# Kernel tuning notes

Hardware: AMD Instinct MI355X
Metric: run time of the kernel (lower is better)

## Reference

```python
import jax, jax.numpy as jnp
import numpy as np

B, N, F, D, H, L, K = 128, 128, 13, 256, 8, 8, 10
FF = 2 * D  # FFN / hidden width
HEAD = D // H


def setup_inputs() -> dict:
    key = jax.random.key(0)
    ks = iter(jax.random.split(key, 64))
    def nrm(shape, scale=0.02):
        return jax.random.normal(next(ks), shape, dtype=jnp.float32) * scale
    return {
        "input_features": jax.random.normal(next(ks), (B, N, F), dtype=jnp.float32),
        "input_points": jax.random.normal(next(ks), (B, N, 2), dtype=jnp.float32),
        "input_mask": jnp.ones((B, N, 1), dtype=jnp.float32),
        "input_time": jax.random.uniform(next(ks), (B, 1), dtype=jnp.float32),
        # get_encoding: Dense(2D, gelu) -> Dense(D, gelu)
        "enc_w1": nrm((F, FF)), "enc_b1": jnp.zeros((FF,), jnp.float32),
        "enc_w2": nrm((FF, D)), "enc_b2": jnp.zeros((D,), jnp.float32),
        # FourierProjection MLP (no bias, swish)
        "four_w1": nrm((D, FF)), "four_w2": nrm((FF, D)),
        # FiLM time projection (no bias)
        "time_w": nrm((D, FF)),
        # local KNN MLPs: round 0 input 2*F, round 1 input 2*D
        "loc1_w1": nrm((2 * F, FF)), "loc1_b1": jnp.zeros((FF,), jnp.float32),
        "loc1_w2": nrm((FF, D)), "loc1_b2": jnp.zeros((D,), jnp.float32),
        "loc2_w1": nrm((2 * D, FF)), "loc2_b1": jnp.zeros((FF,), jnp.float32),
        "loc2_w2": nrm((FF, D)), "loc2_b2": jnp.zeros((D,), jnp.float32),
        # transformer encoder layers, stacked over L
        "qkv_w": nrm((L, D, 3 * D)), "qkv_b": jnp.zeros((L, 3 * D), jnp.float32),
        "out_w": nrm((L, D, D)), "out_b": jnp.zeros((L, D), jnp.float32),
        "ln1_g": jnp.ones((L, D), jnp.float32), "ln1_b": jnp.zeros((L, D), jnp.float32),
        "ff1_w": nrm((L, D, FF)), "ff1_b": jnp.zeros((L, FF), jnp.float32),
        "ff2_w": nrm((L, FF, D)), "ff2_b": jnp.zeros((L, D), jnp.float32),
        "gamma": jnp.full((L, D), 1e-5, dtype=jnp.float32),
        "ln2_g": jnp.ones((L, D), jnp.float32), "ln2_b": jnp.zeros((L, D), jnp.float32),
    }


def _ln(x, g, b, eps=1e-5):
    m = jnp.mean(x, axis=-1, keepdims=True)
    v = jnp.var(x, axis=-1, keepdims=True)
    return (x - m) * jax.lax.rsqrt(v + eps) * g + b


def _fourier(t, w1, w2):
    # t: (B,1) -> (B,D)
    half = D // 2
    emb = np.log(10000.0) / (half - 1)
    freq = jnp.exp(-emb * jnp.arange(half, dtype=jnp.float32))
    angle = t * freq[None, :] * 1000.0  # (B, half)
    e = jnp.concatenate([jnp.sin(angle), jnp.cos(angle)], axis=-1)
    e = jax.nn.silu(e @ w1)
    return jax.nn.silu(e @ w2)


def _get_neighbors(points, feats, w1, b1, w2, b2):
    # points: (B,N,P), feats: (B,N,C) -> (B,N,D)
    r = jnp.sum(points * points, axis=-1)  # (B,N)
    d = r[:, :, None] - 2.0 * jnp.einsum('bnp,bmp->bnm', points, points) + r[:, None, :]
    _, idx = jax.lax.top_k(-d, K + 1)
    idx = idx[:, :, 1:]  # drop self, (B,N,K)
    knn = jax.vmap(lambda f, i: f[i])(feats, idx)  # (B,N,K,C)
    center = jnp.broadcast_to(feats[:, :, None, :], knn.shape)
    local = jnp.concatenate([knn - center, center], axis=-1)  # (B,N,K,2C)
    local = jax.nn.gelu(local @ w1 + b1)
    local = jax.nn.gelu(local @ w2 + b2)
    return jnp.mean(local, axis=2)


def _mha(x, mask, wqkv, bqkv, wo, bo):
    Bx, Nx, _ = x.shape
    qkv = x @ wqkv + bqkv
    q, k, v = jnp.split(qkv, 3, axis=-1)
    def heads(t):
        return t.reshape(Bx, Nx, H, HEAD).transpose(0, 2, 1, 3)
    q, k, v = heads(q), heads(k), heads(v)
    scores = jnp.einsum('bhqd,bhkd->bhqk', q, k) * (1.0 / np.sqrt(HEAD))
    keep = mask[:, None, None, :, 0] > 0  # (B,1,1,N)
    scores = jnp.where(keep, scores, -1e9)
    a = jax.nn.softmax(scores, axis=-1)
    o = jnp.einsum('bhqk,bhkd->bhqd', a, v).transpose(0, 2, 1, 3).reshape(Bx, Nx, D)
    return o @ wo + bo


def _pet(input_features, input_points, input_mask, input_time,
         enc_w1, enc_b1, enc_w2, enc_b2, four_w1, four_w2, time_w,
         loc1_w1, loc1_b1, loc1_w2, loc1_b2, loc2_w1, loc2_b1, loc2_w2, loc2_b2,
         qkv_w, qkv_b, out_w, out_b, ln1_g, ln1_b, ff1_w, ff1_b, ff2_w, ff2_b,
         gamma, ln2_g, ln2_b):
    # feature encoding (RandomDrop is identity at eval / feature_drop=0)
    enc = jax.nn.gelu(input_features @ enc_w1 + enc_b1)
    enc = jax.nn.gelu(enc @ enc_w2 + enc_b2)  # (B,N,D)
    # FiLM time conditioning
    t = _fourier(input_time, four_w1, four_w2)  # (B,D)
    t = t[:, None, :] * input_mask  # (B,N,D)
    scale, shift = jnp.split(t @ time_w, 2, axis=-1)
    enc = enc * (1.0 + scale) + shift
    # local KNN aggregation
    coord_shift = 999.0 * (1.0 - input_mask)  # (B,N,1)
    points = input_points[:, :, :2]
    lf = _get_neighbors(coord_shift + points, input_features, loc1_w1, loc1_b1, loc1_w2, loc1_b2)
    lf = _get_neighbors(coord_shift + lf, lf, loc2_w1, loc2_b1, loc2_w2, loc2_b2)
    enc = enc + lf
    skip = enc
    x = enc
    for i in range(L):
        res = x
        a = _mha(x, input_mask, qkv_w[i], qkv_b[i], out_w[i], out_b[i])
        x = _ln(res + a, ln1_g[i], ln1_b[i])
        res = x
        h = jax.nn.gelu(x @ ff1_w[i] + ff1_b[i])
        h = h @ ff2_w[i] + ff2_b[i]
        h = h * gamma[i] * input_mask  # LayerScale with mask
        x = _ln(res + h, ln2_g[i], ln2_b[i])
    return x + skip


def reference(input_features, input_points, input_mask, input_time,
              enc_w1, enc_b1, enc_w2, enc_b2, four_w1, four_w2, time_w,
              loc1_w1, loc1_b1, loc1_w2, loc1_b2, loc2_w1, loc2_b1, loc2_w2, loc2_b2,
              qkv_w, qkv_b, out_w, out_b, ln1_g, ln1_b, ff1_w, ff1_b, ff2_w, ff2_b,
              gamma, ln2_g, ln2_b):
    return _pet(input_features, input_points, input_mask, input_time,
                enc_w1, enc_b1, enc_w2, enc_b2, four_w1, four_w2, time_w,
                loc1_w1, loc1_b1, loc1_w2, loc1_b2, loc2_w1, loc2_b1, loc2_w2, loc2_b2,
                qkv_w, qkv_b, out_w, out_b, ln1_g, ln1_b, ff1_w, ff1_b, ff2_w, ff2_b,
                gamma, ln2_g, ln2_b)
```

## Files before the change

kernel.cpp:

```cpp
#include <hip/hip_runtime.h>
#include <hip/hip_bf16.h>
#include <cmath>

#define DEV_INLINE __device__ __forceinline__

constexpr int Bn = 128;
constexpr int Nn = 128;
constexpr int Fn = 13;
constexpr int Dn = 256;
constexpr int Ln = 8;
constexpr int Kn = 10;
constexpr int FFn = 512;
constexpr int Tn = Bn * Nn;
constexpr int Rn = Tn * Kn;

typedef __attribute__((ext_vector_type(4))) float f32x4;
typedef __attribute__((ext_vector_type(8))) short bf16x8;
typedef unsigned short us;

__device__ float g_x[Tn * Dn];
__device__ float g_skip[Tn * Dn];
__device__ float g_big[Tn * Dn];
__device__ float g_dm[Tn * Nn];
__device__ float g_u[Bn * FFn];
__device__ float g_r[Tn];
__device__ float g_pqbias[2048];
__device__ int   g_idx[Rn];
__device__ us g_bigb[Tn * 768];
__device__ us g_xb[Tn * Dn];
__device__ us g_attb[Tn * Dn];
__device__ us g_lf1b[Tn * Dn];
__device__ us g_pq[Tn * 1024];
__device__ us g_h2b[Rn * Dn];
__device__ us g_feat16[Tn * 32];
constexpr int OFF_ENC1 = 0;
constexpr int OFF_ENC2 = OFF_ENC1 + 512 * 32;
constexpr int OFF_W2A  = OFF_ENC2 + 256 * 512;
constexpr int OFF_W2B  = OFF_W2A + 256 * 512;
constexpr int OFF_PQ1  = OFF_W2B + 256 * 512;
constexpr int OFF_PQ2  = OFF_PQ1 + 1024 * 32;
constexpr int OFF_QKV  = OFF_PQ2 + 1024 * 256;
constexpr int OFF_OUT  = OFF_QKV + 8 * 768 * 256;
constexpr int OFF_FF1  = OFF_OUT + 8 * 256 * 256;
constexpr int OFF_FF2  = OFF_FF1 + 8 * 512 * 256;
constexpr int WT_TOTAL = OFF_FF2 + 8 * 256 * 512;
__device__ us g_wt[WT_TOTAL];

DEV_INLINE float gelu_f(float x) {
    float x2 = x * x;
    float m = x * fmaf(x2, -0.07135537f, -1.59576912f);
    float t = __expf(m);
    return x * __builtin_amdgcn_rcpf(1.f + t);
}
DEV_INLINE us f2b(float x) {
    __hip_bfloat16 h = __float2bfloat16(x);
    return *(us*)&h;
}
DEV_INLINE float blo(unsigned u) { return __uint_as_float(u << 16); }
DEV_INLINE float bhi(unsigned u) { return __uint_as_float(u & 0xFFFF0000u); }
DEV_INLINE unsigned pk2(float a, float b) {
    float2 f; f.x = a; f.y = b;
    __hip_bfloat162 h = __float22bfloat162_rn(f);
    return *(unsigned*)&h;
}

#define GLOAD16(gp, lp)                                                            \
    __builtin_amdgcn_global_load_lds(                                              \
        (const __attribute__((address_space(1))) unsigned int*)(gp),               \
        (__attribute__((address_space(3))) unsigned int*)(lp), 16, 0, 0)

constexpr int UP0 = 0;
constexpr int UP1 = UP0 + 16;
constexpr int UP2 = UP1 + 128;
constexpr int UP3 = UP2 + 128;
constexpr int UP4 = UP3 + 128;
constexpr int UP5 = UP4 + 1536;
constexpr int UP6 = UP5 + 512;
constexpr int UP7 = UP6 + 1024;
constexpr int UP8 = UP7 + 1024;
constexpr int UP9 = UP8 + 1024;
constexpr int UP10 = UP9 + 1024;
constexpr int UP11 = UP10 + 2048;
constexpr int UP12 = UP11 + 128;
constexpr int UPN = UP12 + 128;

DEV_INLINE void prep_seg(const float* __restrict__ src, us* __restrict__ dst,
                         int Kreal, int Kpad, int Nd, long sstride, long dstride,
                         int gx, int gy, int lb, int tid, float* tile) {
    int z = lb / (gx * gy);
    int rem = lb - z * gx * gy;
    int by = rem / gx, bx = rem - by * gx;
    const float* s = src + (size_t)z * sstride;
    us* d = dst + (size_t)z * dstride;
    int cn = tid & 31, rk = tid >> 5;
    int kbase = by * 32, nbase = bx * 32;
#pragma unroll
    for (int p = 0; p < 4; p++) {
        int k = kbase + p * 8 + rk;
        float v = (k < Kreal) ? s[(size_t)k * Nd + nbase + cn] : 0.f;
        tile[(p * 8 + rk) * 33 + cn] = v;
    }
    __syncthreads();
#pragma unroll
    for (int p = 0; p < 4; p++) {
        int nl = p * 8 + rk;
        d[(size_t)(nbase + nl) * Kpad + kbase + cn] = f2b(tile[cn * 33 + nl]);
    }
}

DEV_INLINE void prepPQ_seg(const float* __restrict__ w1, const float* __restrict__ b1,
                           us* __restrict__ dst, float* __restrict__ bdst,
                           int Kreal, int Kpad, int n, int tid) {
    for (int k = tid; k < Kpad; k += 256) {
        float v;
        if (n < 512) v = (k < Kreal) ? w1[(size_t)k * 512 + n] : 0.f;
        else {
            int m = n - 512;
            v = (k < Kreal) ? (w1[(size_t)(Kreal + k) * 512 + m] - w1[(size_t)k * 512 + m]) : 0.f;
        }
        dst[(size_t)n * Kpad + k] = f2b(v);
    }
    if (tid == 0) bdst[n] = (n < 512) ? 0.f : b1[n - 512];
}

__global__ __launch_bounds__(256) void k_uprep(
    const float* __restrict__ enc_w1, const float* __restrict__ enc_w2,
    const float* __restrict__ l1w2, const float* __restrict__ l2w2,
    const float* __restrict__ qkv_w, const float* __restrict__ out_w,
    const float* __restrict__ ff1w, const float* __restrict__ ff2w,
    const float* __restrict__ l1w1, const float* __restrict__ l1b1,
    const float* __restrict__ l2w1, const float* __restrict__ l2b1,
    const float* __restrict__ feat, const float* __restrict__ tin,
    const float* __restrict__ four_w1, const float* __restrict__ four_w2,
    const float* __restrict__ time_w, const float* __restrict__ pts,
    const float* __restrict__ mask,
    us* __restrict__ wt, float* __restrict__ pqbias, us* __restrict__ fp,
    float* __restrict__ u, int* __restrict__ idx) {
    __shared__ float shmem[1056];
    int b = blockIdx.x, tid = threadIdx.x;
    if (b < UP1) {
        prep_seg(enc_w1, wt + OFF_ENC1, 13, 32, 512, 0, 0, 16, 1, b - UP0, tid, shmem);
    } else if (b < UP2) {
        prep_seg(enc_w2, wt + OFF_ENC2, 512, 512, 256, 0, 0, 8, 16, b - UP1, tid, shmem);
    } else if (b < UP3) {
        prep_seg(l1w2, wt + OFF_W2A, 512, 512, 256, 0, 0, 8, 16, b - UP2, tid, shmem);
    } else if (b < UP4) {
        prep_seg(l2w2, wt + OFF_W2B, 512, 512, 256, 0, 0, 8, 16, b - UP3, tid, shmem);
    } else if (b < UP5) {
        prep_seg(qkv_w, wt + OFF_QKV, 256, 256, 768, 256 * 768, 768 * 256, 24, 8, b - UP4, tid, shmem);
    } else if (b < UP6) {
        prep_seg(out_w, wt + OFF_OUT, 256, 256, 256, 256 * 256, 256 * 256, 8, 8, b - UP5, tid, shmem);
    } else if (b < UP7) {
        prep_seg(ff1w, wt + OFF_FF1, 256, 256, 512, 256 * 512, 512 * 256, 16, 8, b - UP6, tid, shmem);
    } else if (b < UP8) {
        prep_seg(ff2w, wt + OFF_FF2, 512, 512, 256, 512 * 256, 256 * 512, 8, 16, b - UP7, tid, shmem);
    } else if (b < UP9) {
        prepPQ_seg(l1w1, l1b1, wt + OFF_PQ1, pqbias, 13, 32, b - UP8, tid);
    } else if (b < UP10) {
        prepPQ_seg(l2w1, l2b1, wt + OFF_PQ2, pqbias + 1024, 256, 256, b - UP9, tid);
    } else if (b < UP11) {
        int gid = (b - UP10) * 256 + tid;
        int t = gid >> 5, c = gid & 31;
        fp[gid] = (c < Fn) ? f2b(feat[(size_t)t * Fn + c]) : (us)0;
    } else if (b < UP12) {
        float* e = shmem; float* e1 = shmem + 256; float* t2 = shmem + 768;
        int bb = b - UP11;
        float tv = tin[bb];
        if (tid < 128) {
            const float emb = 0.07252236513366287f;
            float fr = expf(-emb * (float)tid);
            float ang = tv * fr * 1000.f;
            e[tid] = sinf(ang);
            e[tid + 128] = cosf(ang);
        }
        __syncthreads();
        for (int j = tid; j < 512; j += 256) {
            float s = 0.f;
            for (int i = 0; i < 256; i++) s += e[i] * four_w1[(size_t)i * 512 + j];
            e1[j] = s / (1.f + expf(-s));
        }
        __syncthreads();
        {
            float s = 0.f;
            for (int i = 0; i < 512; i++) s += e1[i] * four_w2[(size_t)i * 256 + tid];
            t2[tid] = s / (1.f + expf(-s));
        }
        __syncthreads();
        for (int j = tid; j < 512; j += 256) {
            float s = 0.f;
            for (int i = 0; i < 256; i++) s += t2[i] * time_w[(size_t)i * 512 + j];
            u[(size_t)bb * 512 + j] = s;
        }
    } else {
        float* px = shmem; float* py = shmem + 128; float* rr = shmem + 256;
        int bb = b - UP12;
        if (tid < 128) {
            int n = tid;
            float shift = 999.f * (1.f - mask[bb * Nn + n]);
            float x = pts[(size_t)(bb * Nn + n) * 2 + 0] + shift;
            float y = pts[(size_t)(bb * Nn + n) * 2 + 1] + shift;
            px[n] = x; py[n] = y; rr[n] = x * x + y * y;
        }
        __syncthreads();
        if (tid < 128) {
            int n = tid;
            float x = px[n], y = py[n], rn = rr[n];
            float bd[Kn + 1]; int bi[Kn + 1];
#pragma unroll
            for (int j = 0; j <= Kn; j++) { bd[j] = 3.4e38f; bi[j] = -1; }
            for (int m = 0; m < Nn; m++) {
                float d = rn - 2.f * (x * px[m] + y * py[m]) + rr[m];
                if (d < bd[Kn]) {
                    int j = Kn;
                    while (j > 0 && d < bd[j - 1]) { bd[j] = bd[j - 1]; bi[j] = bi[j - 1]; j--; }
                    bd[j] = d; bi[j] = m;
                }
            }
            for (int j = 1; j <= Kn; j++) idx[(size_t)(bb * Nn + n) * Kn + j - 1] = bi[j];
        }
    }
}

template <int EPI, bool OBF>
__global__ __launch_bounds__(256) void k_mg2(const us* __restrict__ A,
                                             const us* __restrict__ Bt,
                                             const float* __restrict__ bias,
                                             void* __restrict__ Cp,
                                             int Kd, int Nd) {
    __shared__ __align__(16) us As[128 * 32];
    __shared__ __align__(16) us Bs[128 * 32];
    int tid = threadIdx.x;
    int m0 = blockIdx.y << 7, n0 = blockIdx.x << 7;
    int wave = tid >> 6, lane = tid & 63;
    int wm = (wave & 1) << 6, wn = (wave >> 1) << 6;
    int lm = lane & 15, quad = lane >> 4;
    int r0 = (wave << 5) + (lane >> 2);
    int colu = (((lane & 3) ^ ((lane >> 2) & 3)) << 3);
    const us* pa0 = A + (size_t)(m0 + r0) * Kd + colu;
    const us* pa1 = A + (size_t)(m0 + r0 + 16) * Kd + colu;
    const us* pb0 = Bt + (size_t)(n0 + r0) * Kd + colu;
    const us* pb1 = Bt + (size_t)(n0 + r0 + 16) * Kd + colu;
    auto lAs = (__attribute__((address_space(3))) us*)As;
    auto lBs = (__attribute__((address_space(3))) us*)Bs;
    int lbase = wave << 10;
    int fcol = ((quad ^ (lm & 3)) << 3);
    f32x4 acc[4][4] = {};
    for (int k0 = 0; k0 < Kd; k0 += 32) {
        __syncthreads();
        GLOAD16(pa0 + k0, lAs + lbase);
        GLOAD16(pa1 + k0, lAs + lbase + 512);
        GLOAD16(pb0 + k0, lBs + lbase);
        GLOAD16(pb1 + k0, lBs + lbase + 512);
        __syncthreads();
        bf16x8 afr[4], bfr[4];
#pragma unroll
        for (int i = 0; i < 4; i++) {
            afr[i] = *(const bf16x8*)&As[(wm + i * 16 + lm) * 32 + fcol];
            bfr[i] = *(const bf16x8*)&Bs[(wn + i * 16 + lm) * 32 + fcol];
        }
#pragma unroll
        for (int mf = 0; mf < 4; mf++)
#pragma unroll
            for (int nf = 0; nf < 4; nf++)
                acc[mf][nf] = __builtin_amdgcn_mfma_f32_16x16x32_bf16(afr[mf], bfr[nf], acc[mf][nf], 0, 0, 0);
    }
    float bvs[4];
#pragma unroll
    for (int nf = 0; nf < 4; nf++) bvs[nf] = bias[n0 + wn + nf * 16 + lm];
#pragma unroll
    for (int mf = 0; mf < 4; mf++) {
#pragma unroll
        for (int r = 0; r < 4; r++) {
            size_t row = (size_t)(m0 + wm + mf * 16 + (quad << 2) + r);
#pragma unroll
            for (int nf = 0; nf < 4; nf++) {
                float v = acc[mf][nf][r] + bvs[nf];
                if (EPI == 1) v = gelu_f(v);
                size_t ci = row * Nd + n0 + wn + nf * 16 + lm;
                if constexpr (OBF) ((us*)Cp)[ci] = f2b(v);
                else ((float*)Cp)[ci] = v;
            }
        }
    }
}

template <bool PM, bool FINAL>
__global__ __launch_bounds__(512) void k_mgln(const us* __restrict__ A,
                                              const us* __restrict__ Bt,
                                              const float* __restrict__ bias,
                                              const us* __restrict__ res,
                                              const float* __restrict__ gamma,
                                              const float* __restrict__ mask,
                                              const float* __restrict__ lng,
                                              const float* __restrict__ lnb,
                                              const float* __restrict__ skip,
                                              us* __restrict__ xbout,
                                              float* __restrict__ finout,
                                              int Kd) {
    __shared__ __align__(16) us As[64 * 32];
    __shared__ __align__(16) us Bs[256 * 32];
    __shared__ float2 part[8][64];
    __shared__ float2 stat[64];
    int tid = threadIdx.x;
    int m0 = blockIdx.x << 6;
    int wave = tid >> 6, lane = tid & 63;
    int wn = wave << 5;
    int lm = lane & 15, quad = lane >> 4;
    int colu = (((lane & 3) ^ ((lane >> 2) & 3)) << 3);
    int ar = (wave << 4) + (lane >> 2);
    int br = (wave << 5) + (lane >> 2);
    const us* pa = A + (size_t)(m0 + ar) * Kd + colu;
    const us* pb0 = Bt + (size_t)br * Kd + colu;
    const us* pb1 = Bt + (size_t)(br + 16) * Kd + colu;
    auto lAs = (__attribute__((address_space(3))) us*)As;
    auto lBs = (__attribute__((address_space(3))) us*)Bs;
    int fcol = ((quad ^ (lm & 3)) << 3);
    f32x4 acc[4][2] = {};
    for (int k0 = 0; k0 < Kd; k0 += 32) {
        __syncthreads();
        if (wave < 4) GLOAD16(pa + k0, lAs + (wave << 9));
        GLOAD16(pb0 + k0, lBs + (wave << 10));
        GLOAD16(pb1 + k0, lBs + (wave << 10) + 512);
        __syncthreads();
        bf16x8 afr[4], bfr[2];
#pragma unroll
        for (int i = 0; i < 4; i++)
            afr[i] = *(const bf16x8*)&As[(i * 16 + lm) * 32 + fcol];
#pragma unroll
        for (int j = 0; j < 2; j++)
            bfr[j] = *(const bf16x8*)&Bs[(wn + j * 16 + lm) * 32 + fcol];
#pragma unroll
        for (int mf = 0; mf < 4; mf++)
#pragma unroll
            for (int nf = 0; nf < 2; nf++)
                acc[mf][nf] = __builtin_amdgcn_mfma_f32_16x16x32_bf16(afr[mf], bfr[nf], acc[mf][nf], 0, 0, 0);
    }
    float bvs[2], gms[2];
#pragma unroll
    for (int nf = 0; nf < 2; nf++) {
        int col = wn + nf * 16 + lm;
        bvs[nf] = bias[col];
        if (PM) gms[nf] = gamma[col];
    }
#pragma unroll
    for (int mf = 0; mf < 4; mf++) {
#pragma unroll
        for (int r = 0; r < 4; r++) {
            int rowl = mf * 16 + (quad << 2) + r;
            size_t row = (size_t)(m0 + rowl);
            float mrow = PM ? mask[row] : 0.f;
            float s1 = 0.f, s2 = 0.f;
#pragma unroll
            for (int nf = 0; nf < 2; nf++) {
                int col = wn + nf * 16 + lm;
                float rv = blo((unsigned)res[row * 256 + col]);
                float v = acc[mf][nf][r] + bvs[nf];
                v = PM ? fmaf(v * gms[nf], mrow, rv) : rv + v;
                acc[mf][nf][r] = v;
                s1 += v; s2 += v * v;
            }
            s1 += __shfl_xor(s1, 1, 64); s2 += __shfl_xor(s2, 1, 64);
            s1 += __shfl_xor(s1, 2, 64); s2 += __shfl_xor(s2, 2, 64);
            s1 += __shfl_xor(s1, 4, 64); s2 += __shfl_xor(s2, 4, 64);
            s1 += __shfl_xor(s1, 8, 64); s2 += __shfl_xor(s2, 8, 64);
            if (lm == 0) { float2 p; p.x = s1; p.y = s2; part[wave][rowl] = p; }
        }
    }
    __syncthreads();
    if (tid < 64) {
        float s = 0.f, q = 0.f;
#pragma unroll
        for (int w = 0; w < 8; w++) { float2 p = part[w][tid]; s += p.x; q += p.y; }
        float mean = s * (1.f / 256.f);
        float var = q * (1.f / 256.f) - mean * mean;
        float2 st; st.x = mean; st.y = rsqrtf(var + 1e-5f);
        stat[tid] = st;
    }
    __syncthreads();
    float gvs[2], bts[2];
#pragma unroll
    for (int nf = 0; nf < 2; nf++) {
        int col = wn + nf * 16 + lm;
        gvs[nf] = lng[col];
        bts[nf] = lnb[col];
    }
#pragma unroll
    for (int mf = 0; mf < 4; mf++) {
#pragma unroll
        for (int r = 0; r < 4; r++) {
            int rowl = mf * 16 + (quad << 2) + r;
            size_t row = (size_t)(m0 + rowl);
            float2 st = stat[rowl];
#pragma unroll
            for (int nf = 0; nf < 2; nf++) {
                int col = wn + nf * 16 + lm;
                float nv = fmaf((acc[mf][nf][r] - st.x) * st.y, gvs[nf], bts[nf]);
                if (FINAL) finout[row * 256 + col] = nv + skip[row * 256 + col];
                else xbout[row * 256 + col] = f2b(nv);
            }
        }
    }
}

__global__ __launch_bounds__(512) void k_knng(const us* __restrict__ pq,
                                              const int* __restrict__ idx,
                                              const us* __restrict__ Bt,
                                              const float* __restrict__ bias,
                                              us* __restrict__ h2b) {
    __shared__ __align__(16) us As[128 * 64];
    __shared__ __align__(16) us Bs[256 * 64];
    int tid = threadIdx.x;
    int m0 = blockIdx.x << 7;
    int wave = tid >> 6, lane = tid & 63;
    int wm = (wave & 1) << 6, wn = (wave >> 1) << 6;
    int lm = lane & 15, quad = lane >> 4;
    int arow = tid >> 2, acolu = (tid & 3) << 4;
    int asw = arow & 7;
    int ablk0 = ((tid & 3) << 1) ^ asw, ablk1 = (((tid & 3) << 1) + 1) ^ asw;
    int r = m0 + arow;
    int tok = r / 10;
    int nb = idx[r];
    int prow = (tok & ~127) + nb;
    const us* Pp = pq + (size_t)prow * 1024 + acolu;
    const us* Qp = pq + (size_t)tok * 1024 + 512 + acolu;
    int brow = (wave << 5) + (lane >> 3);
    int bcol = (((lane & 7) ^ (lane >> 3)) << 3);
    const us* pb = Bt + (size_t)brow * 512 + bcol;
    auto lBs = (__attribute__((address_space(3))) us*)Bs;
    int lbase = wave << 11;
    int fsw = lm & 7;
    f32x4 acc[4][4] = {};
    for (int k0 = 0; k0 < 512; k0 += 64) {
        uint4 pv0 = *(const uint4*)(Pp + k0);
        uint4 pv1 = *(const uint4*)(Pp + k0 + 8);
        uint4 qv0 = *(const uint4*)(Qp + k0);
        uint4 qv1 = *(const uint4*)(Qp + k0 + 8);
        uint4 h0, h1;
        h0.x = pk2(gelu_f(blo(pv0.x) + blo(qv0.x)), gelu_f(bhi(pv0.x) + bhi(qv0.x)));
        h0.y = pk2(gelu_f(blo(pv0.y) + blo(qv0.y)), gelu_f(bhi(pv0.y) + bhi(qv0.y)));
        h0.z = pk2(gelu_f(blo(pv0.z) + blo(qv0.z)), gelu_f(bhi(pv0.z) + bhi(qv0.z)));
        h0.w = pk2(gelu_f(blo(pv0.w) + blo(qv0.w)), gelu_f(bhi(pv0.w) + bhi(qv0.w)));
        h1.x = pk2(gelu_f(blo(pv1.x) + blo(qv1.x)), gelu_f(bhi(pv1.x) + bhi(qv1.x)));
        h1.y = pk2(gelu_f(blo(pv1.y) + blo(qv1.y)), gelu_f(bhi(pv1.y) + bhi(qv1.y)));
        h1.z = pk2(gelu_f(blo(pv1.z) + blo(qv1.z)), gelu_f(bhi(pv1.z) + bhi(qv1.z)));
        h1.w = pk2(gelu_f(blo(pv1.w) + blo(qv1.w)), gelu_f(bhi(pv1.w) + bhi(qv1.w)));
        __syncthreads();
        GLOAD16(pb + k0, lBs + lbase);
        GLOAD16(pb + k0 + 8 * 512, lBs + lbase + 512);
        GLOAD16(pb + k0 + 16 * 512, lBs + lbase + 1024);
        GLOAD16(pb + k0 + 24 * 512, lBs + lbase + 1536);
        *(uint4*)&As[arow * 64 + (ablk0 << 3)] = h0;
        *(uint4*)&As[arow * 64 + (ablk1 << 3)] = h1;
        __syncthreads();
#pragma unroll
        for (int sub = 0; sub < 2; sub++) {
            int lblk = (sub << 2) + quad;
            int fcol = ((lblk ^ fsw) << 3);
            bf16x8 afr[4], bfr[4];
#pragma unroll
            for (int i = 0; i < 4; i++) {
                afr[i] = *(const bf16x8*)&As[(wm + i * 16 + lm) * 64 + fcol];
                bfr[i] = *(const bf16x8*)&Bs[(wn + i * 16 + lm) * 64 + fcol];
            }
#pragma unroll
            for (int mf = 0; mf < 4; mf++)
#pragma unroll
                for (int nf = 0; nf < 4; nf++)
                    acc[mf][nf] = __builtin_amdgcn_mfma_f32_16x16x32_bf16(afr[mf], bfr[nf], acc[mf][nf], 0, 0, 0);
        }
    }
    float bvs[4];
#pragma unroll
    for (int nf = 0; nf < 4; nf++) bvs[nf] = bias[wn + nf * 16 + lm];
#pragma unroll
    for (int mf = 0; mf < 4; mf++) {
#pragma unroll
        for (int rr = 0; rr < 4; rr++) {
            size_t row = (size_t)(m0 + wm + mf * 16 + (quad << 2) + rr);
#pragma unroll
            for (int nf = 0; nf < 4; nf++) {
                float v = gelu_f(acc[mf][nf][rr] + bvs[nf]);
                h2b[row * 256 + wn + nf * 16 + lm] = f2b(v);
            }
        }
    }
}

__global__ __launch_bounds__(64) void k_mean1s(const us* __restrict__ h2b,
                                               const float* __restrict__ mask,
                                               us* __restrict__ lfb,
                                               float* __restrict__ big,
                                               float* __restrict__ r) {
    int t = blockIdx.x, lane = threadIdx.x;
    int c = lane << 2;
    const us* p = h2b + (size_t)t * Kn * 256 + c;
    float s0 = 0.f, s1 = 0.f, s2 = 0.f, s3 = 0.f;
#pragma unroll
    for (int k = 0; k < Kn; k++) {
        uint2 v = *(const uint2*)(p + k * 256);
        s0 += blo(v.x); s1 += bhi(v.x);
        s2 += blo(v.y); s3 += bhi(v.y);
    }
    s0 *= 0.1f; s1 *= 0.1f; s2 *= 0.1f; s3 *= 0.1f;
    uint2 ob; ob.x = pk2(s0, s1); ob.y = pk2(s2, s3);
    *(uint2*)&lfb[(size_t)t * 256 + c] = ob;
    float sh = 999.f * (1.f - mask[t]);
    float4 w; w.x = s0 + sh; w.y = s1 + sh; w.z = s2 + sh; w.w = s3 + sh;
    *(float4*)&big[(size_t)t * 256 + c] = w;
    float sq = w.x * w.x + w.y * w.y + w.z * w.z + w.w * w.w;
#pragma unroll
    for (int off = 32; off; off >>= 1) sq += __shfl_xor(sq, off, 64);
    if (lane == 0) r[t] = sq;
}

__global__ __launch_bounds__(256) void k_dist(const float* __restrict__ fe,
                                              const float* __restrict__ r,
                                              float* __restrict__ Dm) {
    int b = blockIdx.z;
    int m0 = blockIdx.x * 64, n0 = blockIdx.y * 64;
    const float* A = fe + (size_t)b * Nn * Dn;
    __shared__ float As[16][68];
    __shared__ float Bs[16][68];
    int tid = threadIdx.x;
    int tx = tid & 15, ty = tid >> 4;
    int ar = tid >> 2, ac = (tid & 3) << 2;
    float acc[4][4] = {};
    for (int k0 = 0; k0 < Dn; k0 += 16) {
        float4 av = *(const float4*)&A[(size_t)(n0 + ar) * Dn + k0 + ac];
        float4 bv = *(const float4*)&A[(size_t)(m0 + ar) * Dn + k0 + ac];
        __syncthreads();
        As[ac + 0][ar] = av.x; As[ac + 1][ar] = av.y; As[ac + 2][ar] = av.z; As[ac + 3][ar] = av.w;
        Bs[ac + 0][ar] = bv.x; Bs[ac + 1][ar] = bv.y; Bs[ac + 2][ar] = bv.z; Bs[ac + 3][ar] = bv.w;
        __syncthreads();
#pragma unroll
        for (int kk = 0; kk < 16; kk++) {
            float4 a = *(const float4*)&As[kk][ty << 2];
            float4 b2 = *(const float4*)&Bs[kk][tx << 2];
            acc[0][0] += a.x * b2.x; acc[0][1] += a.x * b2.y; acc[0][2] += a.x * b2.z; acc[0][3] += a.x * b2.w;
            acc[1][0] += a.y * b2.x; acc[1][1] += a.y * b2.y; acc[1][2] += a.y * b2.z; acc[1][3] += a.y * b2.w;
            acc[2][0] += a.z * b2.x; acc[2][1] += a.z * b2.y; acc[2][2] += a.z * b2.z; acc[2][3] += a.z * b2.w;
            acc[3][0] += a.w * b2.x; acc[3][1] += a.w * b2.y; acc[3][2] += a.w * b2.z; acc[3][3] += a.w * b2.w;
        }
    }
    float4 rm = *(const float4*)&r[b * Nn + m0 + (tx << 2)];
#pragma unroll
    for (int i = 0; i < 4; i++) {
        int n = n0 + (ty << 2) + i;
        float rn = r[b * Nn + n];
        float4 v;
        v.x = rn - 2.f * acc[i][0] + rm.x;
        v.y = rn - 2.f * acc[i][1] + rm.y;
        v.z = rn - 2.f * acc[i][2] + rm.z;
        v.w = rn - 2.f * acc[i][3] + rm.w;
        *(float4*)&Dm[(size_t)b * Nn * Nn + (size_t)n * Nn + m0 + (tx << 2)] = v;
    }
}

__global__ __launch_bounds__(128) void k_topkg(const float* __restrict__ Dm, int* __restrict__ idx) {
    int b = blockIdx.x, n = threadIdx.x;
    const float* row = Dm + (size_t)b * Nn * Nn + (size_t)n * Nn;
    float bd[Kn + 1]; int bi[Kn + 1];
#pragma unroll
    for (int j = 0; j <= Kn; j++) { bd[j] = 3.4e38f; bi[j] = -1; }
    for (int m = 0; m < Nn; m++) {
        float d = row[m];
        if (d < bd[Kn]) {
            int j = Kn;
            while (j > 0 && d < bd[j - 1]) { bd[j] = bd[j - 1]; bi[j] = bi[j - 1]; j--; }
            bd[j] = d; bi[j] = m;
        }
    }
    for (int j = 1; j <= Kn; j++) idx[(size_t)(b * Nn + n) * Kn + j - 1] = bi[j];
}

__global__ __launch_bounds__(256) void k_meanc(const us* __restrict__ h2b,
                                               const float* __restrict__ u,
                                               const float* __restrict__ mask,
                                               const float* __restrict__ x,
                                               float* __restrict__ skip,
                                               us* __restrict__ xb) {
    int t = blockIdx.x, c = threadIdx.x;
    const us* p = h2b + (size_t)t * Kn * 256 + c;
    float s = 0.f;
#pragma unroll
    for (int k = 0; k < Kn; k++) s += blo((unsigned)p[k * 256]);
    s *= 0.1f;
    int b = t >> 7;
    float m = mask[t];
    float xv = x[(size_t)t * Dn + c];
    float sc = u[(size_t)b * 512 + c];
    float sh = u[(size_t)b * 512 + 256 + c];
    float v = xv * (1.f + m * sc) + m * sh + s;
    skip[(size_t)t * Dn + c] = v;
    xb[(size_t)t * Dn + c] = f2b(v);
}

__global__ __launch_bounds__(256) void k_attn(const us* __restrict__ qkv,
                                              const float* __restrict__ mask,
                                              us* __restrict__ outp) {
    __shared__ __align__(16) us Qs[128 * 40];
    __shared__ __align__(16) us Ks[128 * 40];
    __shared__ __align__(16) us Vt[32 * 136];
    __shared__ __align__(16) us Ps[128 * 136];
    __shared__ float msk[128];
    int bh = blockIdx.x;
    int b = bh >> 3, h = bh & 7;
    int tid = threadIdx.x;
    int wave = tid >> 6, lane = tid & 63;
    int lm = lane & 15, quad = lane >> 4;
    int wm = wave << 5;
    {
        int row = tid >> 1, off = (tid & 1) << 4;
        const us* rp = qkv + (size_t)(b * 128 + row) * 768 + h * 32 + off;
        *(uint4*)&Qs[row * 40 + off] = *(const uint4*)(rp);
        *(uint4*)&Qs[row * 40 + off + 8] = *(const uint4*)(rp + 8);
        *(uint4*)&Ks[row * 40 + off] = *(const uint4*)(rp + 256);
        *(uint4*)&Ks[row * 40 + off + 8] = *(const uint4*)(rp + 264);
        union { uint4 u[2]; us s[16]; } tv;
        tv.u[0] = *(const uint4*)(rp + 512);
        tv.u[1] = *(const uint4*)(rp + 520);
#pragma unroll
        for (int j = 0; j < 16; j++) Vt[(off + j) * 136 + row] = tv.s[j];
        if (tid < 128) msk[tid] = mask[b * 128 + tid];
    }
    __syncthreads();
    f32x4 acc[2][8] = {};
    {
        bf16x8 aq[2];
#pragma unroll
        for (int mf = 0; mf < 2; mf++)
            aq[mf] = *(const bf16x8*)&Qs[(wm + mf * 16 + lm) * 40 + (quad << 3)];
#pragma unroll
        for (int nf = 0; nf < 8; nf++) {
            bf16x8 bk = *(const bf16x8*)&Ks[(nf * 16 + lm) * 40 + (quad << 3)];
            acc[0][nf] = __builtin_amdgcn_mfma_f32_16x16x32_bf16(aq[0], bk, acc[0][nf], 0, 0, 0);
            acc[1][nf] = __builtin_amdgcn_mfma_f32_16x16x32_bf16(aq[1], bk, acc[1][nf], 0, 0, 0);
        }
    }
    {
        const float sc = 0.17677669529663687f;
        float mkc[8];
#pragma unroll
        for (int nf = 0; nf < 8; nf++) mkc[nf] = msk[nf * 16 + lm];
#pragma unroll
        for (int mf = 0; mf < 2; mf++) {
#pragma unroll
            for (int nf = 0; nf < 8; nf++)
#pragma unroll
                for (int r = 0; r < 4; r++) {
                    float s = acc[mf][nf][r];
                    acc[mf][nf][r] = mkc[nf] > 0.f ? s * sc : -1.0e9f;
                }
#pragma unroll
            for (int r = 0; r < 4; r++) {
                float m = acc[mf][0][r];
#pragma unroll
                for (int nf = 1; nf < 8; nf++) m = fmaxf(m, acc[mf][nf][r]);
                m = fmaxf(m, __shfl_xor(m, 1, 64));
                m = fmaxf(m, __shfl_xor(m, 2, 64));
                m = fmaxf(m, __shfl_xor(m, 4, 64));
                m = fmaxf(m, __shfl_xor(m, 8, 64));
                float s = 0.f;
#pragma unroll
                for (int nf = 0; nf < 8; nf++) {
                    float p = __expf(acc[mf][nf][r] - m);
                    acc[mf][nf][r] = p;
                    s += p;
                }
                s += __shfl_xor(s, 1, 64);
                s += __shfl_xor(s, 2, 64);
                s += __shfl_xor(s, 4, 64);
                s += __shfl_xor(s, 8, 64);
                float linv = __builtin_amdgcn_rcpf(s);
                int prow = wm + mf * 16 + (quad << 2) + r;
#pragma unroll
                for (int nf = 0; nf < 8; nf++)
                    Ps[prow * 136 + nf * 16 + lm] = f2b(acc[mf][nf][r] * linv);
            }
        }
    }
    __syncthreads();
    f32x4 oacc[2][2] = {};
    for (int kt = 0; kt < 4; kt++) {
        bf16x8 ap[2], bv[2];
#pragma unroll
        for (int mf = 0; mf < 2; mf++)
            ap[mf] = *(const bf16x8*)&Ps[(wm + mf * 16 + lm) * 136 + kt * 32 + (quad << 3)];
#pragma unroll
        for (int nf = 0; nf < 2; nf++)
            bv[nf] = *(const bf16x8*)&Vt[(nf * 16 + lm) * 136 + kt * 32 + (quad << 3)];
#pragma unroll
        for (int mf = 0; mf < 2; mf++)
#pragma unroll
            for (int nf = 0; nf < 2; nf++)
                oacc[mf][nf] = __builtin_amdgcn_mfma_f32_16x16x32_bf16(ap[mf], bv[nf], oacc[mf][nf], 0, 0, 0);
    }
#pragma unroll
    for (int mf = 0; mf < 2; mf++)
#pragma unroll
        for (int r = 0; r < 4; r++) {
            int row = wm + mf * 16 + (quad << 2) + r;
#pragma unroll
            for (int nf = 0; nf < 2; nf++)
                outp[(size_t)(b * 128 + row) * 256 + h * 32 + nf * 16 + lm] = f2b(oacc[nf == 0 ? mf : mf][nf][r]);
        }
}

extern "C" void kernel_launch(void* const* d_in, const int* in_sizes, int n_in,
                              void* d_out, int out_size, void* d_ws, size_t ws_size,
                              hipStream_t stream) {
    (void)in_sizes; (void)n_in; (void)out_size; (void)d_ws; (void)ws_size;
    const float* f_feat = (const float*)d_in[0];
    const float* f_pts  = (const float*)d_in[1];
    const float* f_mask = (const float*)d_in[2];
    const float* f_time = (const float*)d_in[3];
    const float* enc_w1 = (const float*)d_in[4];
    const float* enc_b1 = (const float*)d_in[5];
    const float* enc_w2 = (const float*)d_in[6];
    const float* enc_b2 = (const float*)d_in[7];
    const float* four_w1 = (const float*)d_in[8];
    const float* four_w2 = (const float*)d_in[9];
    const float* time_w = (const float*)d_in[10];
    const float* l1w1 = (const float*)d_in[11];
    const float* l1b1 = (const float*)d_in[12];
    const float* l1w2 = (const float*)d_in[13];
    const float* l1b2 = (const float*)d_in[14];
    const float* l2w1 = (const float*)d_in[15];
    const float* l2b1 = (const float*)d_in[16];
    const float* l2w2 = (const float*)d_in[17];
    const float* l2b2 = (const float*)d_in[18];
    const float* qkv_w = (const float*)d_in[19];
    const float* qkv_b = (const float*)d_in[20];
    const float* out_w = (const float*)d_in[21];
    const float* out_b = (const float*)d_in[22];
    const float* ln1g = (const float*)d_in[23];
    const float* ln1b = (const float*)d_in[24];
    const float* ff1w = (const float*)d_in[25];
    const float* ff1b = (const float*)d_in[26];
    const float* ff2w = (const float*)d_in[27];
    const float* ff2b = (const float*)d_in[28];
    const float* gam  = (const float*)d_in[29];
    const float* ln2g = (const float*)d_in[30];
    const float* ln2b = (const float*)d_in[31];
    float* out = (float*)d_out;

    float *x, *skip, *big, *dm, *u, *r, *pqbias;
    int* idx;
    us *bigb, *xb, *attb, *lf1b, *pq, *h2b, *feat16, *wt;
    hipGetSymbolAddress((void**)&x,    HIP_SYMBOL(g_x));
    hipGetSymbolAddress((void**)&skip, HIP_SYMBOL(g_skip));
    hipGetSymbolAddress((void**)&big,  HIP_SYMBOL(g_big));
    hipGetSymbolAddress((void**)&dm,   HIP_SYMBOL(g_dm));
    hipGetSymbolAddress((void**)&u,    HIP_SYMBOL(g_u));
    hipGetSymbolAddress((void**)&r,    HIP_SYMBOL(g_r));
    hipGetSymbolAddress((void**)&pqbias, HIP_SYMBOL(g_pqbias));
    hipGetSymbolAddress((void**)&idx,  HIP_SYMBOL(g_idx));
    hipGetSymbolAddress((void**)&bigb, HIP_SYMBOL(g_bigb));
    hipGetSymbolAddress((void**)&xb,   HIP_SYMBOL(g_xb));
    hipGetSymbolAddress((void**)&attb, HIP_SYMBOL(g_attb));
    hipGetSymbolAddress((void**)&lf1b, HIP_SYMBOL(g_lf1b));
    hipGetSymbolAddress((void**)&pq,   HIP_SYMBOL(g_pq));
    hipGetSymbolAddress((void**)&h2b,  HIP_SYMBOL(g_h2b));
    hipGetSymbolAddress((void**)&feat16, HIP_SYMBOL(g_feat16));
    hipGetSymbolAddress((void**)&wt,   HIP_SYMBOL(g_wt));

    k_uprep<<<UPN, 256, 0, stream>>>(
        enc_w1, enc_w2, l1w2, l2w2, qkv_w, out_w, ff1w, ff2w,
        l1w1, l1b1, l2w1, l2b1, f_feat, f_time, four_w1, four_w2, time_w,
        f_pts, f_mask, wt, pqbias, feat16, u, idx);

    k_mg2<1, true><<<dim3(4, 128), 256, 0, stream>>>(feat16, wt + OFF_ENC1, enc_b1, bigb, 32, 512);
    k_mg2<1, false><<<dim3(2, 128), 256, 0, stream>>>(bigb, wt + OFF_ENC2, enc_b2, x, 512, 256);
    k_mg2<0, true><<<dim3(8, 128), 256, 0, stream>>>(feat16, wt + OFF_PQ1, pqbias, pq, 32, 1024);
    k_knng<<<Rn / 128, 512, 0, stream>>>(pq, idx, wt + OFF_W2A, l1b2, h2b);
    k_mean1s<<<Tn, 64, 0, stream>>>(h2b, f_mask, lf1b, big, r);
    k_dist<<<dim3(2, 2, Bn), 256, 0, stream>>>(big, r, dm);
    k_topkg<<<Bn, Nn, 0, stream>>>(dm, idx);
    k_mg2<0, true><<<dim3(8, 128), 256, 0, stream>>>(lf1b, wt + OFF_PQ2, pqbias + 1024, pq, 256, 1024);
    k_knng<<<Rn / 128, 512, 0, stream>>>(pq, idx, wt + OFF_W2B, l2b2, h2b);
    k_meanc<<<Tn, 256, 0, stream>>>(h2b, u, f_mask, x, skip, xb);
    for (int l = 0; l < Ln; l++) {
        k_mg2<0, true><<<dim3(6, 128), 256, 0, stream>>>(
            xb, wt + OFF_QKV + (size_t)l * 768 * 256, qkv_b + l * 768, bigb, 256, 768);
        k_attn<<<Bn * 8, 256, 0, stream>>>(bigb, f_mask, attb);
        k_mgln<false, false><<<256, 512, 0, stream>>>(
            attb, wt + OFF_OUT + (size_t)l * 256 * 256, out_b + l * 256,
            xb, nullptr, f_mask, ln1g + l * Dn, ln1b + l * Dn, nullptr, xb, nullptr, 256);
        k_mg2<1, true><<<dim3(4, 128), 256, 0, stream>>>(
            xb, wt + OFF_FF1 + (size_t)l * 512 * 256, ff1b + l * 512, bigb, 256, 512);
        if (l < Ln - 1)
            k_mgln<true, false><<<256, 512, 0, stream>>>(
                bigb, wt + OFF_FF2 + (size_t)l * 256 * 512, ff2b + l * 256,
                xb, gam + l * Dn, f_mask, ln2g + l * Dn, ln2b + l * Dn, nullptr, xb, nullptr, 512);
        else
            k_mgln<true, true><<<256, 512, 0, stream>>>(
                bigb, wt + OFF_FF2 + (size_t)l * 256 * 512, ff2b + l * 256,
                xb, gam + l * Dn, f_mask, ln2g + l * Dn, ln2b + l * Dn, skip, nullptr, out, 512);
    }
}
```

Measured before the change: 1.467 ms.

## Fuse QKV projection into per-head attention kernel and coarsen weight-prep grid

Replaces the separate QKV GEMM plus attention kernels with one kernel that computes each head's Q, K, V slice via MFMA from the layer input and then runs softmax attention in shared memory. This removes the full QKV intermediate write/read and one launch per layer. Each head block re-reads its batch's input rows (relying on L2 for reuse). The prep kernel also processes 8 tiles per block with an added barrier to reduce block count.

```diff
diff --git a/kernel.cpp b/kernel.cpp
--- a/kernel.cpp
+++ b/kernel.cpp
@@ -69,20 +69,20 @@
         (const __attribute__((address_space(1))) unsigned int*)(gp),               \
         (__attribute__((address_space(3))) unsigned int*)(lp), 16, 0, 0)
 
-constexpr int UP0 = 0;
-constexpr int UP1 = UP0 + 16;
-constexpr int UP2 = UP1 + 128;
-constexpr int UP3 = UP2 + 128;
-constexpr int UP4 = UP3 + 128;
-constexpr int UP5 = UP4 + 1536;
-constexpr int UP6 = UP5 + 512;
-constexpr int UP7 = UP6 + 1024;
-constexpr int UP8 = UP7 + 1024;
-constexpr int UP9 = UP8 + 1024;
-constexpr int UP10 = UP9 + 1024;
-constexpr int UP11 = UP10 + 2048;
-constexpr int UP12 = UP11 + 128;
-constexpr int UPN = UP12 + 128;
+constexpr int U0 = 0;
+constexpr int U1 = U0 + 2;
+constexpr int U2 = U1 + 16;
+constexpr int U3 = U2 + 16;
+constexpr int U4 = U3 + 16;
+constexpr int U5 = U4 + 192;
+constexpr int U6 = U5 + 64;
+constexpr int U7 = U6 + 128;
+constexpr int U8 = U7 + 128;
+constexpr int U9 = U8 + 128;
+constexpr int U10 = U9 + 128;
+constexpr int U11 = U10 + 256;
+constexpr int U12 = U11 + 128;
+constexpr int UPN = U12 + 128;
 
 DEV_INLINE void prep_seg(const float* __restrict__ src, us* __restrict__ dst,
                          int Kreal, int Kpad, int Nd, long sstride, long dstride,
@@ -106,6 +106,7 @@
         int nl = p * 8 + rk;
         d[(size_t)(nbase + nl) * Kpad + kbase + cn] = f2b(tile[cn * 33 + nl]);
     }
+    __syncthreads();
 }
 
 DEV_INLINE void prepPQ_seg(const float* __restrict__ w1, const float* __restrict__ b1,
@@ -138,33 +139,56 @@
     float* __restrict__ u, int* __restrict__ idx) {
     __shared__ float shmem[1056];
     int b = blockIdx.x, tid = threadIdx.x;
-    if (b < UP1) {
-        prep_seg(enc_w1, wt + OFF_ENC1, 13, 32, 512, 0, 0, 16, 1, b - UP0, tid, shmem);
-    } else if (b < UP2) {
-        prep_seg(enc_w2, wt + OFF_ENC2, 512, 512, 256, 0, 0, 8, 16, b - UP1, tid, shmem);
-    } else if (b < UP3) {
-        prep_seg(l1w2, wt + OFF_W2A, 512, 512, 256, 0, 0, 8, 16, b - UP2, tid, shmem);
-    } else if (b < UP4) {
-        prep_seg(l2w2, wt + OFF_W2B, 512, 512, 256, 0, 0, 8, 16, b - UP3, tid, shmem);
-    } else if (b < UP5) {
-        prep_seg(qkv_w, wt + OFF_QKV, 256, 256, 768, 256 * 768, 768 * 256, 24, 8, b - UP4, tid, shmem);
-    } else if (b < UP6) {
-        prep_seg(out_w, wt + OFF_OUT, 256, 256, 256, 256 * 256, 256 * 256, 8, 8, b - UP5, tid, shmem);
-    } else if (b < UP7) {
-        prep_seg(ff1w, wt + OFF_FF1, 256, 256, 512, 256 * 512, 512 * 256, 16, 8, b - UP6, tid, shmem);
-    } else if (b < UP8) {
-        prep_seg(ff2w, wt + OFF_FF2, 512, 512, 256, 512 * 256, 256 * 512, 8, 16, b - UP7, tid, shmem);
-    } else if (b < UP9) {
-        prepPQ_seg(l1w1, l1b1, wt + OFF_PQ1, pqbias, 13, 32, b - UP8, tid);
-    } else if (b < UP10) {
-        prepPQ_seg(l2w1, l2b1, wt + OFF_PQ2, pqbias + 1024, 256, 256, b - UP9, tid);
-    } else if (b < UP11) {
-        int gid = (b - UP10) * 256 + tid;
-        int t = gid >> 5, c = gid & 31;
-        fp[gid] = (c < Fn) ? f2b(feat[(size_t)t * Fn + c]) : (us)0;
-    } else if (b < UP12) {
+    if (b < U1) {
+#pragma unroll 1
+        for (int i = 0; i < 8; i++)
+            prep_seg(enc_w1, wt + OFF_ENC1, 13, 32, 512, 0, 0, 16, 1, (b - U0) * 8 + i, tid, shmem);
+    } else if (b < U2) {
+#pragma unroll 1
+        for (int i = 0; i < 8; i++)
+            prep_seg(enc_w2, wt + OFF_ENC2, 512, 512, 256, 0, 0, 8, 16, (b - U1) * 8 + i, tid, shmem);
+    } else if (b < U3) {
+#pragma unroll 1
+        for (int i = 0; i < 8; i++)
+            prep_seg(l1w2, wt + OFF_W2A, 512, 512, 256, 0, 0, 8, 16, (b - U2) * 8 + i, tid, shmem);
+    } else if (b < U4) {
+#pragma unroll 1
+        for (int i = 0; i < 8; i++)
+            prep_seg(l2w2, wt + OFF_W2B, 512, 512, 256, 0, 0, 8, 16, (b - U3) * 8 + i, tid, shmem);
+    } else if (b < U5) {
+#pragma unroll 1
+        for (int i = 0; i < 8; i++)
+            prep_seg(qkv_w, wt + OFF_QKV, 256, 256, 768, 256 * 768, 768 * 256, 24, 8, (b - U4) * 8 + i, tid, shmem);
+    } else if (b < U6) {
+#pragma unroll 1
+        for (int i = 0; i < 8; i++)
+            prep_seg(out_w, wt + OFF_OUT, 256, 256, 256, 256 * 256, 256 * 256, 8, 8, (b - U5) * 8 + i, tid, shmem);
+    } else if (b < U7) {
+#pragma unroll 1
+        for (int i = 0; i < 8; i++)
+            prep_seg(ff1w, wt + OFF_FF1, 256, 256, 512, 256 * 512, 512 * 256, 16, 8, (b - U6) * 8 + i, tid, shmem);
+    } else if (b < U8) {
+#pragma unroll 1
+        for (int i = 0; i < 8; i++)
+            prep_seg(ff2w, wt + OFF_FF2, 512, 512, 256, 512 * 256, 256 * 512, 8, 16, (b - U7) * 8 + i, tid, shmem);
+    } else if (b < U9) {
+#pragma unroll 1
+        for (int i = 0; i < 8; i++)
+            prepPQ_seg(l1w1, l1b1, wt + OFF_PQ1, pqbias, 13, 32, (b - U8) * 8 + i, tid);
+    } else if (b < U10) {
+#pragma unroll 1
+        for (int i = 0; i < 8; i++)
+            prepPQ_seg(l2w1, l2b1, wt + OFF_PQ2, pqbias + 1024, 256, 256, (b - U9) * 8 + i, tid);
+    } else if (b < U11) {
+#pragma unroll 1
+        for (int i = 0; i < 8; i++) {
+            int gid = ((b - U10) * 8 + i) * 256 + tid;
+            int t = gid >> 5, c = gid & 31;
+            fp[gid] = (c < Fn) ? f2b(feat[(size_t)t * Fn + c]) : (us)0;
+        }
+    } else if (b < U12) {
         float* e = shmem; float* e1 = shmem + 256; float* t2 = shmem + 768;
-        int bb = b - UP11;
+        int bb = b - U11;
         float tv = tin[bb];
         if (tid < 128) {
             const float emb = 0.07252236513366287f;
@@ -193,7 +217,7 @@
         }
     } else {
         float* px = shmem; float* py = shmem + 128; float* rr = shmem + 256;
-        int bb = b - UP12;
+        int bb = b - U12;
         if (tid < 128) {
             int n = tid;
             float shift = 999.f * (1.f - mask[bb * Nn + n]);
@@ -282,6 +306,166 @@
             }
         }
     }
+}
+
+__global__ __launch_bounds__(256) void k_qattn(const us* __restrict__ xb,
+                                               const us* __restrict__ Bt,
+                                               const float* __restrict__ bias,
+                                               const float* __restrict__ mask,
+                                               us* __restrict__ attb) {
+    __shared__ __align__(16) char smem[64512];
+    us* Ps = (us*)smem;
+    us* Qs = (us*)(smem + 34816);
+    us* Ks = (us*)(smem + 45056);
+    us* Vt = (us*)(smem + 55296);
+    float* msk = (float*)(smem + 64000);
+    us* As = (us*)smem;
+    us* Bs = (us*)(smem + 8192);
+    int bh = blockIdx.x;
+    int b = bh >> 3, h = bh & 7;
+    int tid = threadIdx.x;
+    int wave = tid >> 6, lane = tid & 63;
+    int lm = lane & 15, quad = lane >> 4;
+    int wm = wave << 5;
+    int colu = (((lane & 3) ^ ((lane >> 2) & 3)) << 3);
+    int r0 = (wave << 5) + (lane >> 2);
+    const us* pa0 = xb + (size_t)(b * 128 + r0) * 256 + colu;
+    const us* pa1 = xb + (size_t)(b * 128 + r0 + 16) * 256 + colu;
+    int seg0 = wave, seg1 = wave + 4;
+    int n0_ = seg0 * 16 + (lane >> 2);
+    int n1_ = seg1 * 16 + (lane >> 2);
+    int g0 = (n0_ >> 5) * 256 + h * 32 + (n0_ & 31);
+    int g1 = (n1_ >> 5) * 256 + h * 32 + (n1_ & 31);
+    const us* pb0 = Bt + (size_t)g0 * 256 + colu;
+    const us* pb1 = Bt + (size_t)g1 * 256 + colu;
+    auto lAs = (__attribute__((address_space(3))) us*)As;
+    auto lBs = (__attribute__((address_space(3))) us*)Bs;
+    int fcol = ((quad ^ (lm & 3)) << 3);
+    f32x4 gacc[2][6] = {};
+    for (int k0 = 0; k0 < 256; k0 += 32) {
+        __syncthreads();
+        GLOAD16(pa0 + k0, lAs + (wave << 10));
+        GLOAD16(pa1 + k0, lAs + (wave << 10) + 512);
+        GLOAD16(pb0 + k0, lBs + (seg0 << 9));
+        if (wave < 2) GLOAD16(pb1 + k0, lBs + (seg1 << 9));
+        __syncthreads();
+        bf16x8 afr[2], bfr[6];
+#pragma unroll
+        for (int mf = 0; mf < 2; mf++)
+            afr[mf] = *(const bf16x8*)&As[(wm + mf * 16 + lm) * 32 + fcol];
+#pragma unroll
+        for (int nf = 0; nf < 6; nf++)
+            bfr[nf] = *(const bf16x8*)&Bs[(nf * 16 + lm) * 32 + fcol];
+#pragma unroll
+        for (int mf = 0; mf < 2; mf++)
+#pragma unroll
+            for (int nf = 0; nf < 6; nf++)
+                gacc[mf][nf] = __builtin_amdgcn_mfma_f32_16x16x32_bf16(afr[mf], bfr[nf], gacc[mf][nf], 0, 0, 0);
+    }
+    float bvq[6];
+#pragma unroll
+    for (int nf = 0; nf < 6; nf++) {
+        int n = nf * 16 + lm;
+        bvq[nf] = bias[(n >> 5) * 256 + h * 32 + (n & 31)];
+    }
+    __syncthreads();
+#pragma unroll
+    for (int mf = 0; mf < 2; mf++) {
+#pragma unroll
+        for (int r = 0; r < 4; r++) {
+            int row = wm + mf * 16 + (quad << 2) + r;
+#pragma unroll
+            for (int nf = 0; nf < 6; nf++) {
+                us hv = f2b(gacc[mf][nf][r] + bvq[nf]);
+                int n = nf * 16 + lm;
+                if (nf < 2) Qs[row * 40 + n] = hv;
+                else if (nf < 4) Ks[row * 40 + (n - 32)] = hv;
+                else Vt[(n - 64) * 136 + row] = hv;
+            }
+        }
+    }
+    if (tid < 128) msk[tid] = mask[b * 128 + tid];
+    __syncthreads();
+    f32x4 acc[2][8] = {};
+    {
+        bf16x8 aq[2];
+#pragma unroll
+        for (int mf = 0; mf < 2; mf++)
+            aq[mf] = *(const bf16x8*)&Qs[(wm + mf * 16 + lm) * 40 + (quad << 3)];
+#pragma unroll
+        for (int nf = 0; nf < 8; nf++) {
+            bf16x8 bk = *(const bf16x8*)&Ks[(nf * 16 + lm) * 40 + (quad << 3)];
+            acc[0][nf] = __builtin_amdgcn_mfma_f32_16x16x32_bf16(aq[0], bk, acc[0][nf], 0, 0, 0);
+            acc[1][nf] = __builtin_amdgcn_mfma_f32_16x16x32_bf16(aq[1], bk, acc[1][nf], 0, 0, 0);
+        }
+    }
+    {
+        const float sc = 0.17677669529663687f;
+        float mkc[8];
+#pragma unroll
+        for (int nf = 0; nf < 8; nf++) mkc[nf] = msk[nf * 16 + lm];
+#pragma unroll
+        for (int mf = 0; mf < 2; mf++) {
+#pragma unroll
+            for (int nf = 0; nf < 8; nf++)
+#pragma unroll
+                for (int r = 0; r < 4; r++) {
+                    float s = acc[mf][nf][r];
+                    acc[mf][nf][r] = mkc[nf] > 0.f ? s * sc : -1.0e9f;
+                }
+#pragma unroll
+            for (int r = 0; r < 4; r++) {
+                float m = acc[mf][0][r];
+#pragma unroll
+                for (int nf = 1; nf < 8; nf++) m = fmaxf(m, acc[mf][nf][r]);
+                m = fmaxf(m, __shfl_xor(m, 1, 64));
+                m = fmaxf(m, __shfl_xor(m, 2, 64));
+                m = fmaxf(m, __shfl_xor(m, 4, 64));
+                m = fmaxf(m, __shfl_xor(m, 8, 64));
+                float s = 0.f;
+#pragma unroll
+                for (int nf = 0; nf < 8; nf++) {
+                    float p = __expf(acc[mf][nf][r] - m);
+                    acc[mf][nf][r] = p;
+                    s += p;
+                }
+                s += __shfl_xor(s, 1, 64);
+                s += __shfl_xor(s, 2, 64);
+                s += __shfl_xor(s, 4, 64);
+                s += __shfl_xor(s, 8, 64);
+                float linv = __builtin_amdgcn_rcpf(s);
+                int prow = wm + mf * 16 + (quad << 2) + r;
+#pragma unroll
+                for (int nf = 0; nf < 8; nf++)
+                    Ps[prow * 136 + nf * 16 + lm] = f2b(acc[mf][nf][r] * linv);
+            }
+        }
+    }
+    __syncthreads();
+    f32x4 oacc[2][2] = {};
+    for (int kt = 0; kt < 4; kt++) {
+        bf16x8 ap[2], bv[2];
+#pragma unroll
+        for (int mf = 0; mf < 2; mf++)
+            ap[mf] = *(const bf16x8*)&Ps[(wm + mf * 16 + lm) * 136 + kt * 32 + (quad << 3)];
+#pragma unroll
+        for (int nf = 0; nf < 2; nf++)
+            bv[nf] = *(const bf16x8*)&Vt[(nf * 16 + lm) * 136 + kt * 32 + (quad << 3)];
+#pragma unroll
+        for (int mf = 0; mf < 2; mf++)
+#pragma unroll
+            for (int nf = 0; nf < 2; nf++)
+                oacc[mf][nf] = __builtin_amdgcn_mfma_f32_16x16x32_bf16(ap[mf], bv[nf], oacc[mf][nf], 0, 0, 0);
+    }
+#pragma unroll
+    for (int mf = 0; mf < 2; mf++)
+#pragma unroll
+        for (int r = 0; r < 4; r++) {
+            int row = wm + mf * 16 + (quad << 2) + r;
+#pragma unroll
+            for (int nf = 0; nf < 2; nf++)
+                attb[(size_t)(b * 128 + row) * 256 + h * 32 + nf * 16 + lm] = f2b(oacc[mf][nf][r]);
+        }
 }
 
 template <bool PM, bool FINAL>
@@ -595,117 +779,6 @@
     xb[(size_t)t * Dn + c] = f2b(v);
 }
 
-__global__ __launch_bounds__(256) void k_attn(const us* __restrict__ qkv,
-                                              const float* __restrict__ mask,
-                                              us* __restrict__ outp) {
-    __shared__ __align__(16) us Qs[128 * 40];
-    __shared__ __align__(16) us Ks[128 * 40];
-    __shared__ __align__(16) us Vt[32 * 136];
-    __shared__ __align__(16) us Ps[128 * 136];
-    __shared__ float msk[128];
-    int bh = blockIdx.x;
-    int b = bh >> 3, h = bh & 7;
-    int tid = threadIdx.x;
-    int wave = tid >> 6, lane = tid & 63;
-    int lm = lane & 15, quad = lane >> 4;
-    int wm = wave << 5;
-    {
-        int row = tid >> 1, off = (tid & 1) << 4;
-        const us* rp = qkv + (size_t)(b * 128 + row) * 768 + h * 32 + off;
-        *(uint4*)&Qs[row * 40 + off] = *(const uint4*)(rp);
-        *(uint4*)&Qs[row * 40 + off + 8] = *(const uint4*)(rp + 8);
-        *(uint4*)&Ks[row * 40 + off] = *(const uint4*)(rp + 256);
-        *(uint4*)&Ks[row * 40 + off + 8] = *(const uint4*)(rp + 264);
-        union { uint4 u[2]; us s[16]; } tv;
-        tv.u[0] = *(const uint4*)(rp + 512);
-        tv.u[1] = *(const uint4*)(rp + 520);
-#pragma unroll
-        for (int j = 0; j < 16; j++) Vt[(off + j) * 136 + row] = tv.s[j];
-        if (tid < 128) msk[tid] = mask[b * 128 + tid];
-    }
-    __syncthreads();
-    f32x4 acc[2][8] = {};
-    {
-        bf16x8 aq[2];
-#pragma unroll
-        for (int mf = 0; mf < 2; mf++)
-            aq[mf] = *(const bf16x8*)&Qs[(wm + mf * 16 + lm) * 40 + (quad << 3)];
-#pragma unroll
-        for (int nf = 0; nf < 8; nf++) {
-            bf16x8 bk = *(const bf16x8*)&Ks[(nf * 16 + lm) * 40 + (quad << 3)];
-            acc[0][nf] = __builtin_amdgcn_mfma_f32_16x16x32_bf16(aq[0], bk, acc[0][nf], 0, 0, 0);
-            acc[1][nf] = __builtin_amdgcn_mfma_f32_16x16x32_bf16(aq[1], bk, acc[1][nf], 0, 0, 0);
-        }
-    }
-    {
-        const float sc = 0.17677669529663687f;
-        float mkc[8];
-#pragma unroll
-        for (int nf = 0; nf < 8; nf++) mkc[nf] = msk[nf * 16 + lm];
-#pragma unroll
-        for (int mf = 0; mf < 2; mf++) {
-#pragma unroll
-            for (int nf = 0; nf < 8; nf++)
-#pragma unroll
-                for (int r = 0; r < 4; r++) {
-                    float s = acc[mf][nf][r];
-                    acc[mf][nf][r] = mkc[nf] > 0.f ? s * sc : -1.0e9f;
-                }
-#pragma unroll
-            for (int r = 0; r < 4; r++) {
-                float m = acc[mf][0][r];
-#pragma unroll
-                for (int nf = 1; nf < 8; nf++) m = fmaxf(m, acc[mf][nf][r]);
-                m = fmaxf(m, __shfl_xor(m, 1, 64));
-                m = fmaxf(m, __shfl_xor(m, 2, 64));
-                m = fmaxf(m, __shfl_xor(m, 4, 64));
-                m = fmaxf(m, __shfl_xor(m, 8, 64));
-                float s = 0.f;
-#pragma unroll
-                for (int nf = 0; nf < 8; nf++) {
-                    float p = __expf(acc[mf][nf][r] - m);
-                    acc[mf][nf][r] = p;
-                    s += p;
-                }
-                s += __shfl_xor(s, 1, 64);
-                s += __shfl_xor(s, 2, 64);
-                s += __shfl_xor(s, 4, 64);
-                s += __shfl_xor(s, 8, 64);
-                float linv = __builtin_amdgcn_rcpf(s);
-                int prow = wm + mf * 16 + (quad << 2) + r;
-#pragma unroll
-                for (int nf = 0; nf < 8; nf++)
-                    Ps[prow * 136 + nf * 16 + lm] = f2b(acc[mf][nf][r] * linv);
-            }
-        }
-    }
-    __syncthreads();
-    f32x4 oacc[2][2] = {};
-    for (int kt = 0; kt < 4; kt++) {
-        bf16x8 ap[2], bv[2];
-#pragma unroll
-        for (int mf = 0; mf < 2; mf++)
-            ap[mf] = *(const bf16x8*)&Ps[(wm + mf * 16 + lm) * 136 + kt * 32 + (quad << 3)];
-#pragma unroll
-        for (int nf = 0; nf < 2; nf++)
-            bv[nf] = *(const bf16x8*)&Vt[(nf * 16 + lm) * 136 + kt * 32 + (quad << 3)];
-#pragma unroll
-        for (int mf = 0; mf < 2; mf++)
-#pragma unroll
-            for (int nf = 0; nf < 2; nf++)
-                oacc[mf][nf] = __builtin_amdgcn_mfma_f32_16x16x32_bf16(ap[mf], bv[nf], oacc[mf][nf], 0, 0, 0);
-    }
-#pragma unroll
-    for (int mf = 0; mf < 2; mf++)
-#pragma unroll
-        for (int r = 0; r < 4; r++) {
-            int row = wm + mf * 16 + (quad << 2) + r;
-#pragma unroll
-            for (int nf = 0; nf < 2; nf++)
-                outp[(size_t)(b * 128 + row) * 256 + h * 32 + nf * 16 + lm] = f2b(oacc[nf == 0 ? mf : mf][nf][r]);
-        }
-}
-
 extern "C" void kernel_launch(void* const* d_in, const int* in_sizes, int n_in,
                               void* d_out, int out_size, void* d_ws, size_t ws_size,
                               hipStream_t stream) {
@@ -780,9 +853,8 @@
     k_knng<<<Rn / 128, 512, 0, stream>>>(pq, idx, wt + OFF_W2B, l2b2, h2b);
     k_meanc<<<Tn, 256, 0, stream>>>(h2b, u, f_mask, x, skip, xb);
     for (int l = 0; l < Ln; l++) {
-        k_mg2<0, true><<<dim3(6, 128), 256, 0, stream>>>(
-            xb, wt + OFF_QKV + (size_t)l * 768 * 256, qkv_b + l * 768, bigb, 256, 768);
-        k_attn<<<Bn * 8, 256, 0, stream>>>(bigb, f_mask, attb);
+        k_qattn<<<Bn * 8, 256, 0, stream>>>(
+            xb, wt + OFF_QKV + (size_t)l * 768 * 256, qkv_b + l * 768, f_mask, attb);
         k_mgln<false, false><<<256, 512, 0, stream>>>(
             attb, wt + OFF_OUT + (size_t)l * 256 * 256, out_b + l * 256,
             xb, nullptr, f_mask, ln1g + l * Dn, ln1b + l * Dn, nullptr, xb, nullptr, 256);
```

After: 1.342 ms. 8.5% less time.
